# Performance work log

Measured on AMD Instinct MI355X. Metric: run time of the kernel, lower is better.

## Reference

```python
import jax, jax.numpy as jnp
import numpy as np

IN_FEATURES = 4096
OUT_FEATURES = 16384
BATCH, SEQ = 4, 2048


def setup_inputs() -> dict:
    key = jax.random.key(0)
    k_x, k_w, k_b = jax.random.split(key, 3)
    x = jax.random.normal(k_x, (BATCH, SEQ, IN_FEATURES), dtype=jnp.float32)
    # int8-valued quantized weight stored as int32 for portability (values in [-128, 127])
    weight_quantized = jax.random.randint(k_w, (OUT_FEATURES, IN_FEATURES), -128, 128, dtype=jnp.int32)
    weight_scale = jnp.float32(0.01)        # scalar scale (symmetric quant)
    weight_zero_point = jnp.float32(0.0)    # scalar zero point
    bias = jax.random.normal(k_b, (OUT_FEATURES,), dtype=jnp.float32)
    return {
        "x": x,
        "weight_quantized": weight_quantized,
        "weight_scale": weight_scale,
        "weight_zero_point": weight_zero_point,
        "bias": bias,
    }


def reference(x, weight_quantized, weight_scale, weight_zero_point, bias):
    # dequantize: (q - zero_point) * scale  -> fp32 weight [out, in]
    weight = (weight_quantized.astype(jnp.float32) - weight_zero_point) * weight_scale
    # F.linear: y = x @ W^T + b ; x: [b, s, in], W: [out, in] -> y: [b, s, out]
    return jnp.einsum("bsi,oi->bso", x, weight) + bias
```

## Files before the change

### kernel.cpp

```cpp
#include <hip/hip_runtime.h>
#include <hip/hip_bf16.h>
#include <cstdint>


#define M_DIM 8192
#define N_DIM 16384
#define K_DIM 4096
#define BK    128
#define NT    (K_DIM / BK)

using i32x4  = __attribute__((ext_vector_type(4))) int;
using i32x16 = __attribute__((ext_vector_type(16))) int;

__global__ __launch_bounds__(256) void quant_x_kernel(const float* __restrict__ x,
                                                      signed char* __restrict__ xq,
                                                      float* __restrict__ rs1,
                                                      float* __restrict__ rs2) {
    const int row = blockIdx.x;
    const float* xr = x + (size_t)row * K_DIM;
    const int tid = threadIdx.x;

    float4 v[4];
    float amax = 0.f;
    #pragma unroll
    for (int j = 0; j < 4; ++j) {
        v[j] = *(const float4*)(xr + j * 1024 + tid * 4);
        amax = fmaxf(amax, fmaxf(fmaxf(fabsf(v[j].x), fabsf(v[j].y)),
                                 fmaxf(fabsf(v[j].z), fabsf(v[j].w))));
    }
    #pragma unroll
    for (int off = 32; off > 0; off >>= 1)
        amax = fmaxf(amax, __shfl_xor(amax, off));
    __shared__ float smax[4];
    __shared__ int   ssum[4];
    const int wv = tid >> 6, ln = tid & 63;
    if (ln == 0) smax[wv] = amax;
    __syncthreads();
    amax = fmaxf(fmaxf(smax[0], smax[1]), fmaxf(smax[2], smax[3]));
    const float s   = amax * (1.0f / 127.0f);
    const float inv = amax > 0.f ? 127.0f / amax : 0.f;

    int sum = 0;
    #pragma unroll
    for (int j = 0; j < 4; ++j) {
        int q0 = (int)__builtin_rintf(v[j].x * inv);
        int q1 = (int)__builtin_rintf(v[j].y * inv);
        int q2 = (int)__builtin_rintf(v[j].z * inv);
        int q3 = (int)__builtin_rintf(v[j].w * inv);
        sum += q0 + q1 + q2 + q3;
        int packed = (q0 & 255) | ((q1 & 255) << 8) | ((q2 & 255) << 16) | ((q3 & 255) << 24);
        *(int*)(xq + (size_t)row * K_DIM + j * 1024 + tid * 4) = packed;
    }
    #pragma unroll
    for (int off = 32; off > 0; off >>= 1)
        sum += __shfl_xor(sum, off);
    if (ln == 0) ssum[wv] = sum;
    __syncthreads();
    if (tid == 0) {
        int t = ssum[0] + ssum[1] + ssum[2] + ssum[3];
        rs1[row] = s;
        rs2[row] = s * (float)t;
    }
}

__global__ void quant_w_kernel(const int* __restrict__ q, signed char* __restrict__ o,
                               long long n) {
    long long i = ((long long)blockIdx.x * blockDim.x + threadIdx.x) * 4;
    const long long stride = (long long)gridDim.x * blockDim.x * 4;
    for (; i < n; i += stride) {
        int4 v = *(const int4*)(q + i);
        int packed = (v.x & 255) | ((v.y & 255) << 8) | ((v.z & 255) << 16) | ((v.w & 255) << 24);
        *(int*)(o + i) = packed;
    }
}

#define SB() __builtin_amdgcn_sched_barrier(0)

__device__ __forceinline__ void barrier_() {
    SB();
    asm volatile("" ::: "memory");
    __builtin_amdgcn_s_barrier();
    asm volatile("" ::: "memory");
    SB();
}

__device__ __forceinline__ void stage_half8(const signed char* g0, unsigned char* l0) {
    __builtin_amdgcn_global_load_lds((const __attribute__((address_space(1))) void*)g0,
                                     (__attribute__((address_space(3))) void*)l0, 16, 0, 0);
    __builtin_amdgcn_global_load_lds(
        (const __attribute__((address_space(1))) void*)(g0 + (size_t)64 * K_DIM),
        (__attribute__((address_space(3))) void*)(l0 + 8192), 16, 0, 0);
}

__global__ __launch_bounds__(512, 2) void gemm_i8_kernel(const signed char* __restrict__ A,
                                                         const signed char* __restrict__ B,
                                                         const float* __restrict__ rs1,
                                                         const float* __restrict__ rs2,
                                                         const float* __restrict__ scale,
                                                         const float* __restrict__ zpp,
                                                         const float* __restrict__ bias,
                                                         float* __restrict__ C) {
    extern __shared__ unsigned char smem[];

    const int tid  = threadIdx.x;
    const int wave = tid >> 6;
    const int lane = tid & 63;
    const int fr = lane & 31, klo = lane >> 5;
    const int wr = wave >> 2, wc = wave & 3;

    const int nwg = (M_DIM / 256) * (N_DIM / 256);
    const int cpx = nwg >> 3;
    const int swz = (blockIdx.x & 7) * cpx + (blockIdx.x >> 3);
    const int ntn = N_DIM / 256;
    const int tileRow = (swz / ntn) * 256;
    const int tileCol = (swz % ntn) * 256;

    const size_t goff = (size_t)(tid >> 3) * K_DIM + (((tid & 7) ^ ((tid >> 3) & 7)) * 16);
    const signed char* Au  = A + (size_t)tileRow * K_DIM + goff;
    const signed char* Bu  = B + (size_t)tileCol * K_DIM + goff;
    const signed char* AuH = Au + (size_t)128 * K_DIM;
    const signed char* BuH = Bu + (size_t)128 * K_DIM;

    const int rA = wr * 128 + fr;
    const int rB = wc * 64 + fr;
    const int aoffB = rA * 128;
    const int boffB = 32768 + rB * 128;
    int cA[4], cB[4];
    #pragma unroll
    for (int ks = 0; ks < 4; ++ks) {
        cA[ks] = ((ks * 2 + klo) ^ (rA & 7)) * 16;
        cB[ks] = ((ks * 2 + klo) ^ (rB & 7)) * 16;
    }

    i32x16 acc[4][2] = {};
    i32x4 arA[2][4], arB[2][4], b0r[4], b1r[4];

    {
        unsigned char* w0 = smem + wave * 1024;
        unsigned char* w1 = smem + 65536 + wave * 1024;
        stage_half8(Au,  w0);
        stage_half8(AuH, w0 + 16384);
        stage_half8(Bu,  w0 + 32768);
        stage_half8(BuH, w0 + 49152);
        stage_half8(Bu + BK, w1 + 32768);
        stage_half8(Au + BK, w1);
    }
    SB();
    asm volatile("s_waitcnt vmcnt(4)" ::: "memory");
    barrier_();
    #pragma unroll
    for (int m = 0; m < 2; ++m)
        #pragma unroll
        for (int ks = 0; ks < 4; ++ks)
            arA[m][ks] = *(const i32x4*)(smem + aoffB + m * 4096 + cA[ks]);
    #pragma unroll
    for (int ks = 0; ks < 4; ++ks)
        b0r[ks] = *(const i32x4*)(smem + boffB + cB[ks]);
    SB();

    for (int t = 0; t < NT; ++t) {
        const unsigned char* sbr = smem + (t & 1) * 65536;
        const unsigned char* nxr = smem + ((t + 1) & 1) * 65536;
        unsigned char* sbw = smem + (t & 1) * 65536 + wave * 1024;
        unsigned char* nxw = smem + ((t + 1) & 1) * 65536 + wave * 1024;
        const int kn1 = (t + 1) * BK, kn2 = (t + 2) * BK;

        if (t + 1 < NT) stage_half8(AuH + kn1, nxw + 16384);
        #pragma unroll
        for (int ks = 0; ks < 4; ++ks)
            b1r[ks] = *(const i32x4*)(sbr + boffB + 4096 + cB[ks]);
        SB();
        asm volatile("s_waitcnt lgkmcnt(4)" ::: "memory");
        SB();
        __builtin_amdgcn_s_setprio(1);
        #pragma unroll
        for (int m = 0; m < 2; ++m)
            #pragma unroll
            for (int ks = 0; ks < 4; ++ks)
                acc[m][0] = __builtin_amdgcn_mfma_i32_32x32x32_i8(arA[m][ks], b0r[ks], acc[m][0], 0, 0, 0);
        __builtin_amdgcn_s_setprio(0);
        barrier_();

        if (t + 1 < NT) stage_half8(BuH + kn1, nxw + 49152);
        #pragma unroll
        for (int m = 0; m < 2; ++m)
            #pragma unroll
            for (int ks = 0; ks < 4; ++ks)
                arB[m][ks] = *(const i32x4*)(sbr + aoffB + (m + 2) * 4096 + cA[ks]);
        SB();
        asm volatile("s_waitcnt lgkmcnt(8)" ::: "memory");
        SB();
        __builtin_amdgcn_s_setprio(1);
        #pragma unroll
        for (int m = 0; m < 2; ++m)
            #pragma unroll
            for (int ks = 0; ks < 4; ++ks)
                acc[m][1] = __builtin_amdgcn_mfma_i32_32x32x32_i8(arA[m][ks], b1r[ks], acc[m][1], 0, 0, 0);
        __builtin_amdgcn_s_setprio(0);
        barrier_();

        if (t + 2 < NT) stage_half8(Bu + kn2, sbw + 32768);
        SB();
        asm volatile("s_waitcnt lgkmcnt(0)" ::: "memory");
        SB();
        __builtin_amdgcn_s_setprio(1);
        #pragma unroll
        for (int m = 0; m < 2; ++m)
            #pragma unroll
            for (int ks = 0; ks < 4; ++ks)
                acc[m + 2][1] = __builtin_amdgcn_mfma_i32_32x32x32_i8(arB[m][ks], b1r[ks], acc[m + 2][1], 0, 0, 0);
        __builtin_amdgcn_s_setprio(0);
        SB();
        if (t + 2 < NT) {
            asm volatile("s_waitcnt vmcnt(2)" ::: "memory");
        } else {
            asm volatile("s_waitcnt vmcnt(0)" ::: "memory");
        }
        barrier_();

        if (t + 1 < NT) {
            #pragma unroll
            for (int m = 0; m < 2; ++m)
                #pragma unroll
                for (int ks = 0; ks < 4; ++ks)
                    arA[m][ks] = *(const i32x4*)(nxr + aoffB + m * 4096 + cA[ks]);
        }
        if (t + 2 < NT) stage_half8(Au + kn2, sbw);
        SB();
        __builtin_amdgcn_s_setprio(1);
        #pragma unroll
        for (int m = 0; m < 2; ++m)
            #pragma unroll
            for (int ks = 0; ks < 4; ++ks)
                acc[m + 2][0] = __builtin_amdgcn_mfma_i32_32x32x32_i8(arB[m][ks], b0r[ks], acc[m + 2][0], 0, 0, 0);
        __builtin_amdgcn_s_setprio(0);
        if (t + 1 < NT) {
            #pragma unroll
            for (int ks = 0; ks < 4; ++ks)
                b0r[ks] = *(const i32x4*)(nxr + boffB + cB[ks]);
        }
        SB();
        barrier_();
    }

    const float sw  = scale[0];
    const float zpv = zpp[0];
    const float bv0 = bias[tileCol + wc * 64 + fr];
    const float bv1 = bias[tileCol + wc * 64 + 32 + fr];
    #pragma unroll
    for (int m = 0; m < 4; ++m) {
        #pragma unroll
        for (int r = 0; r < 16; ++r) {
            const int grow = tileRow + wr * 128 + m * 32 + (r & 3) + 8 * (r >> 2) + 4 * klo;
            const float f1 = rs1[grow] * sw;
            const float f2 = zpv * rs2[grow] * sw;
            const int gc0 = tileCol + wc * 64 + fr;
            C[(size_t)grow * N_DIM + gc0]      = f1 * (float)acc[m][0][r] - f2 + bv0;
            C[(size_t)grow * N_DIM + gc0 + 32] = f1 * (float)acc[m][1][r] - f2 + bv1;
        }
    }
}

__global__ void gemm_naive(const float* __restrict__ x, const int* __restrict__ wq,
                           const float* __restrict__ sp, const float* __restrict__ zp,
                           const float* __restrict__ bias, float* __restrict__ out) {
    __shared__ float sX[32][33];
    __shared__ float sW[32][33];
    const float s = sp[0], z = zp[0];
    const int tx = threadIdx.x & 15, ty = threadIdx.x >> 4;
    const int row0 = blockIdx.y * 32, col0 = blockIdx.x * 32;
    float acc[2][2] = {};
    for (int k0 = 0; k0 < K_DIM; k0 += 32) {
        for (int i = threadIdx.x; i < 32 * 32; i += 256) {
            int r = i >> 5, c = i & 31;
            sX[r][c] = x[(size_t)(row0 + r) * K_DIM + k0 + c];
            sW[r][c] = ((float)wq[(size_t)(col0 + r) * K_DIM + k0 + c] - z) * s;
        }
        __syncthreads();
        #pragma unroll
        for (int k = 0; k < 32; ++k) {
            float xa0 = sX[ty * 2][k], xa1 = sX[ty * 2 + 1][k];
            float wb0 = sW[tx * 2][k], wb1 = sW[tx * 2 + 1][k];
            acc[0][0] += xa0 * wb0; acc[0][1] += xa0 * wb1;
            acc[1][0] += xa1 * wb0; acc[1][1] += xa1 * wb1;
        }
        __syncthreads();
    }
    #pragma unroll
    for (int i = 0; i < 2; ++i)
        #pragma unroll
        for (int j = 0; j < 2; ++j)
            out[(size_t)(row0 + ty * 2 + i) * N_DIM + (col0 + tx * 2 + j)] =
                acc[i][j] + bias[col0 + tx * 2 + j];
}

extern "C" void kernel_launch(void* const* d_in, const int* in_sizes, int n_in,
                              void* d_out, int out_size, void* d_ws, size_t ws_size,
                              hipStream_t stream) {
    const float* x     = (const float*)d_in[0];
    const int*   wq    = (const int*)d_in[1];
    const float* scale = (const float*)d_in[2];
    const float* zp    = (const float*)d_in[3];
    const float* bias  = (const float*)d_in[4];
    float* out = (float*)d_out;

    const size_t offXq = 0;
    const size_t offWq = (size_t)M_DIM * K_DIM;
    const size_t offR1 = offWq + (size_t)N_DIM * K_DIM;
    const size_t offR2 = offR1 + (size_t)M_DIM * sizeof(float);
    const size_t need  = offR2 + (size_t)M_DIM * sizeof(float);

    if (ws_size >= need) {
        signed char* xq  = (signed char*)d_ws + offXq;
        signed char* wq8 = (signed char*)d_ws + offWq;
        float* rs1 = (float*)((char*)d_ws + offR1);
        float* rs2 = (float*)((char*)d_ws + offR2);
        quant_x_kernel<<<M_DIM, 256, 0, stream>>>(x, xq, rs1, rs2);
        quant_w_kernel<<<4096, 256, 0, stream>>>(wq, wq8, (long long)N_DIM * K_DIM);
        (void)hipFuncSetAttribute((const void*)gemm_i8_kernel,
                                  hipFuncAttributeMaxDynamicSharedMemorySize, 131072);
        gemm_i8_kernel<<<(M_DIM / 256) * (N_DIM / 256), 512, 131072, stream>>>(
            xq, wq8, rs1, rs2, scale, zp, bias, out);
    } else {
        dim3 grid(N_DIM / 32, M_DIM / 32);
        gemm_naive<<<grid, 256, 0, stream>>>(x, wq, scale, zp, bias, out);
    }
}
```

Measured before the change: 684.9 us.

## Use 4-wave workgroups with 128x128 per-wave tiles in int8 GEMM

Halves the workgroup from 512 to 256 threads, so each wave computes a 128x128 output subtile (4x4 MFMA accumulators) instead of 128x64. Each LDS fragment load now feeds more MFMAs, raising register-level reuse and cutting LDS read traffic per FLOP, and each thread issues four async global-to-LDS loads per stage. The tile-to-block swizzle is also changed to walk rows first within each column group. The cost is doubled accumulator registers, which limits occupancy to one workgroup per CU and leaves fewer waves to hide latency.

Measured after the change: 767.4 us. 12.0% more time.

```diff
diff --git a/kernel.cpp b/kernel.cpp
--- a/kernel.cpp
+++ b/kernel.cpp
@@ -84,15 +84,15 @@
     SB();
 }
 
-__device__ __forceinline__ void stage_half8(const signed char* g0, unsigned char* l0) {
-    __builtin_amdgcn_global_load_lds((const __attribute__((address_space(1))) void*)g0,
-                                     (__attribute__((address_space(3))) void*)l0, 16, 0, 0);
-    __builtin_amdgcn_global_load_lds(
-        (const __attribute__((address_space(1))) void*)(g0 + (size_t)64 * K_DIM),
-        (__attribute__((address_space(3))) void*)(l0 + 8192), 16, 0, 0);
-}
-
-__global__ __launch_bounds__(512, 2) void gemm_i8_kernel(const signed char* __restrict__ A,
+__device__ __forceinline__ void stage_half4(const signed char* g0, unsigned char* l0) {
+    #pragma unroll
+    for (int j = 0; j < 4; ++j)
+        __builtin_amdgcn_global_load_lds(
+            (const __attribute__((address_space(1))) void*)(g0 + (size_t)(j * 32) * K_DIM),
+            (__attribute__((address_space(3))) void*)(l0 + j * 4096), 16, 0, 0);
+}
+
+__global__ __launch_bounds__(256, 1) void gemm_i8_kernel(const signed char* __restrict__ A,
                                                          const signed char* __restrict__ B,
                                                          const float* __restrict__ rs1,
                                                          const float* __restrict__ rs2,
@@ -106,14 +106,11 @@
     const int wave = tid >> 6;
     const int lane = tid & 63;
     const int fr = lane & 31, klo = lane >> 5;
-    const int wr = wave >> 2, wc = wave & 3;
-
-    const int nwg = (M_DIM / 256) * (N_DIM / 256);
-    const int cpx = nwg >> 3;
-    const int swz = (blockIdx.x & 7) * cpx + (blockIdx.x >> 3);
-    const int ntn = N_DIM / 256;
-    const int tileRow = (swz / ntn) * 256;
-    const int tileCol = (swz % ntn) * 256;
+    const int wr = wave >> 1, wc = wave & 1;
+
+    const int swz = (blockIdx.x & 7) * 256 + (blockIdx.x >> 3);
+    const int tileRow = (swz & 31) * 256;
+    const int tileCol = (swz >> 5) * 256;
 
     const size_t goff = (size_t)(tid >> 3) * K_DIM + (((tid & 7) ^ ((tid >> 3) & 7)) * 16);
     const signed char* Au  = A + (size_t)tileRow * K_DIM + goff;
@@ -121,41 +118,39 @@
     const signed char* AuH = Au + (size_t)128 * K_DIM;
     const signed char* BuH = Bu + (size_t)128 * K_DIM;
 
-    const int rA = wr * 128 + fr;
-    const int rB = wc * 64 + fr;
-    const int aoffB = rA * 128;
-    const int boffB = 32768 + rB * 128;
-    int cA[4], cB[4];
-    #pragma unroll
-    for (int ks = 0; ks < 4; ++ks) {
-        cA[ks] = ((ks * 2 + klo) ^ (rA & 7)) * 16;
-        cB[ks] = ((ks * 2 + klo) ^ (rB & 7)) * 16;
-    }
-
-    i32x16 acc[4][2] = {};
-    i32x4 arA[2][4], arB[2][4], b0r[4], b1r[4];
+    const int aoffB = wr * 16384 + fr * 128;
+    const int boffB = 32768 + wc * 16384 + fr * 128;
+    int c[4];
+    #pragma unroll
+    for (int ks = 0; ks < 4; ++ks)
+        c[ks] = ((ks * 2 + klo) ^ (fr & 7)) * 16;
+
+    i32x16 acc[4][4] = {};
+    i32x4 arA[2][4], arB[2][4], b0r[2][4], b1r[2][4];
 
     {
         unsigned char* w0 = smem + wave * 1024;
         unsigned char* w1 = smem + 65536 + wave * 1024;
-        stage_half8(Au,  w0);
-        stage_half8(AuH, w0 + 16384);
-        stage_half8(Bu,  w0 + 32768);
-        stage_half8(BuH, w0 + 49152);
-        stage_half8(Bu + BK, w1 + 32768);
-        stage_half8(Au + BK, w1);
+        stage_half4(Au,  w0);
+        stage_half4(AuH, w0 + 16384);
+        stage_half4(Bu,  w0 + 32768);
+        stage_half4(BuH, w0 + 49152);
+        stage_half4(Bu + BK, w1 + 32768);
+        stage_half4(Au + BK, w1);
     }
     SB();
-    asm volatile("s_waitcnt vmcnt(4)" ::: "memory");
+    asm volatile("s_waitcnt vmcnt(8)" ::: "memory");
     barrier_();
     #pragma unroll
     for (int m = 0; m < 2; ++m)
         #pragma unroll
         for (int ks = 0; ks < 4; ++ks)
-            arA[m][ks] = *(const i32x4*)(smem + aoffB + m * 4096 + cA[ks]);
-    #pragma unroll
-    for (int ks = 0; ks < 4; ++ks)
-        b0r[ks] = *(const i32x4*)(smem + boffB + cB[ks]);
+            arA[m][ks] = *(const i32x4*)(smem + aoffB + m * 4096 + c[ks]);
+    #pragma unroll
+    for (int n = 0; n < 2; ++n)
+        #pragma unroll
+        for (int ks = 0; ks < 4; ++ks)
+            b0r[n][ks] = *(const i32x4*)(smem + boffB + n * 4096 + c[ks]);
     SB();
 
     for (int t = 0; t < NT; ++t) {
@@ -165,55 +160,63 @@
         unsigned char* nxw = smem + ((t + 1) & 1) * 65536 + wave * 1024;
         const int kn1 = (t + 1) * BK, kn2 = (t + 2) * BK;
 
-        if (t + 1 < NT) stage_half8(AuH + kn1, nxw + 16384);
-        #pragma unroll
-        for (int ks = 0; ks < 4; ++ks)
-            b1r[ks] = *(const i32x4*)(sbr + boffB + 4096 + cB[ks]);
-        SB();
-        asm volatile("s_waitcnt lgkmcnt(4)" ::: "memory");
+        if (t + 1 < NT) stage_half4(AuH + kn1, nxw + 16384);
+        #pragma unroll
+        for (int n = 0; n < 2; ++n)
+            #pragma unroll
+            for (int ks = 0; ks < 4; ++ks)
+                b1r[n][ks] = *(const i32x4*)(sbr + boffB + (n + 2) * 4096 + c[ks]);
+        SB();
+        asm volatile("s_waitcnt lgkmcnt(8)" ::: "memory");
         SB();
         __builtin_amdgcn_s_setprio(1);
         #pragma unroll
-        for (int m = 0; m < 2; ++m)
-            #pragma unroll
-            for (int ks = 0; ks < 4; ++ks)
-                acc[m][0] = __builtin_amdgcn_mfma_i32_32x32x32_i8(arA[m][ks], b0r[ks], acc[m][0], 0, 0, 0);
+        for (int ks = 0; ks < 4; ++ks)
+            #pragma unroll
+            for (int m = 0; m < 2; ++m)
+                #pragma unroll
+                for (int n = 0; n < 2; ++n)
+                    acc[m][n] = __builtin_amdgcn_mfma_i32_32x32x32_i8(arA[m][ks], b0r[n][ks], acc[m][n], 0, 0, 0);
         __builtin_amdgcn_s_setprio(0);
         barrier_();
 
-        if (t + 1 < NT) stage_half8(BuH + kn1, nxw + 49152);
+        if (t + 1 < NT) stage_half4(BuH + kn1, nxw + 49152);
         #pragma unroll
         for (int m = 0; m < 2; ++m)
             #pragma unroll
             for (int ks = 0; ks < 4; ++ks)
-                arB[m][ks] = *(const i32x4*)(sbr + aoffB + (m + 2) * 4096 + cA[ks]);
+                arB[m][ks] = *(const i32x4*)(sbr + aoffB + (m + 2) * 4096 + c[ks]);
         SB();
         asm volatile("s_waitcnt lgkmcnt(8)" ::: "memory");
         SB();
         __builtin_amdgcn_s_setprio(1);
         #pragma unroll
-        for (int m = 0; m < 2; ++m)
-            #pragma unroll
-            for (int ks = 0; ks < 4; ++ks)
-                acc[m][1] = __builtin_amdgcn_mfma_i32_32x32x32_i8(arA[m][ks], b1r[ks], acc[m][1], 0, 0, 0);
+        for (int ks = 0; ks < 4; ++ks)
+            #pragma unroll
+            for (int m = 0; m < 2; ++m)
+                #pragma unroll
+                for (int n = 0; n < 2; ++n)
+                    acc[m][n + 2] = __builtin_amdgcn_mfma_i32_32x32x32_i8(arA[m][ks], b1r[n][ks], acc[m][n + 2], 0, 0, 0);
         __builtin_amdgcn_s_setprio(0);
         barrier_();
 
-        if (t + 2 < NT) stage_half8(Bu + kn2, sbw + 32768);
+        if (t + 2 < NT) stage_half4(Bu + kn2, sbw + 32768);
         SB();
         asm volatile("s_waitcnt lgkmcnt(0)" ::: "memory");
         SB();
         __builtin_amdgcn_s_setprio(1);
         #pragma unroll
-        for (int m = 0; m < 2; ++m)
-            #pragma unroll
-            for (int ks = 0; ks < 4; ++ks)
-                acc[m + 2][1] = __builtin_amdgcn_mfma_i32_32x32x32_i8(arB[m][ks], b1r[ks], acc[m + 2][1], 0, 0, 0);
+        for (int ks = 0; ks < 4; ++ks)
+            #pragma unroll
+            for (int m = 0; m < 2; ++m)
+                #pragma unroll
+                for (int n = 0; n < 2; ++n)
+                    acc[m + 2][n + 2] = __builtin_amdgcn_mfma_i32_32x32x32_i8(arB[m][ks], b1r[n][ks], acc[m + 2][n + 2], 0, 0, 0);
         __builtin_amdgcn_s_setprio(0);
         SB();
         if (t + 2 < NT) {
-            asm volatile("s_waitcnt vmcnt(2)" ::: "memory");
-        } else {
+            asm volatile("s_waitcnt vmcnt(4)" ::: "memory");
+        } else if (t + 1 < NT) {
             asm volatile("s_waitcnt vmcnt(0)" ::: "memory");
         }
         barrier_();
@@ -223,21 +226,25 @@
             for (int m = 0; m < 2; ++m)
                 #pragma unroll
                 for (int ks = 0; ks < 4; ++ks)
-                    arA[m][ks] = *(const i32x4*)(nxr + aoffB + m * 4096 + cA[ks]);
-        }
-        if (t + 2 < NT) stage_half8(Au + kn2, sbw);
+                    arA[m][ks] = *(const i32x4*)(nxr + aoffB + m * 4096 + c[ks]);
+        }
+        if (t + 2 < NT) stage_half4(Au + kn2, sbw);
         SB();
         __builtin_amdgcn_s_setprio(1);
         #pragma unroll
-        for (int m = 0; m < 2; ++m)
-            #pragma unroll
-            for (int ks = 0; ks < 4; ++ks)
-                acc[m + 2][0] = __builtin_amdgcn_mfma_i32_32x32x32_i8(arB[m][ks], b0r[ks], acc[m + 2][0], 0, 0, 0);
+        for (int ks = 0; ks < 4; ++ks)
+            #pragma unroll
+            for (int m = 0; m < 2; ++m)
+                #pragma unroll
+                for (int n = 0; n < 2; ++n)
+                    acc[m + 2][n] = __builtin_amdgcn_mfma_i32_32x32x32_i8(arB[m][ks], b0r[n][ks], acc[m + 2][n], 0, 0, 0);
         __builtin_amdgcn_s_setprio(0);
         if (t + 1 < NT) {
             #pragma unroll
-            for (int ks = 0; ks < 4; ++ks)
-                b0r[ks] = *(const i32x4*)(nxr + boffB + cB[ks]);
+            for (int n = 0; n < 2; ++n)
+                #pragma unroll
+                for (int ks = 0; ks < 4; ++ks)
+                    b0r[n][ks] = *(const i32x4*)(nxr + boffB + n * 4096 + c[ks]);
         }
         SB();
         barrier_();
@@ -245,8 +252,10 @@
 
     const float sw  = scale[0];
     const float zpv = zpp[0];
-    const float bv0 = bias[tileCol + wc * 64 + fr];
-    const float bv1 = bias[tileCol + wc * 64 + 32 + fr];
+    float bv[4];
+    #pragma unroll
+    for (int n = 0; n < 4; ++n)
+        bv[n] = bias[tileCol + wc * 128 + n * 32 + fr];
     #pragma unroll
     for (int m = 0; m < 4; ++m) {
         #pragma unroll
@@ -254,9 +263,10 @@
             const int grow = tileRow + wr * 128 + m * 32 + (r & 3) + 8 * (r >> 2) + 4 * klo;
             const float f1 = rs1[grow] * sw;
             const float f2 = zpv * rs2[grow] * sw;
-            const int gc0 = tileCol + wc * 64 + fr;
-            C[(size_t)grow * N_DIM + gc0]      = f1 * (float)acc[m][0][r] - f2 + bv0;
-            C[(size_t)grow * N_DIM + gc0 + 32] = f1 * (float)acc[m][1][r] - f2 + bv1;
+            float* Crow = C + (size_t)grow * N_DIM + tileCol + wc * 128 + fr;
+            #pragma unroll
+            for (int n = 0; n < 4; ++n)
+                Crow[n * 32] = f1 * (float)acc[m][n][r] - f2 + bv[n];
         }
     }
 }
@@ -272,9 +282,9 @@
     float acc[2][2] = {};
     for (int k0 = 0; k0 < K_DIM; k0 += 32) {
         for (int i = threadIdx.x; i < 32 * 32; i += 256) {
-            int r = i >> 5, c = i & 31;
-            sX[r][c] = x[(size_t)(row0 + r) * K_DIM + k0 + c];
-            sW[r][c] = ((float)wq[(size_t)(col0 + r) * K_DIM + k0 + c] - z) * s;
+            int r = i >> 5, cc2 = i & 31;
+            sX[r][cc2] = x[(size_t)(row0 + r) * K_DIM + k0 + cc2];
+            sW[r][cc2] = ((float)wq[(size_t)(col0 + r) * K_DIM + k0 + cc2] - z) * s;
         }
         __syncthreads();
         #pragma unroll
@@ -319,7 +329,7 @@
         quant_w_kernel<<<4096, 256, 0, stream>>>(wq, wq8, (long long)N_DIM * K_DIM);
         (void)hipFuncSetAttribute((const void*)gemm_i8_kernel,
                                   hipFuncAttributeMaxDynamicSharedMemorySize, 131072);
-        gemm_i8_kernel<<<(M_DIM / 256) * (N_DIM / 256), 512, 131072, stream>>>(
+        gemm_i8_kernel<<<(M_DIM / 256) * (N_DIM / 256), 256, 131072, stream>>>(
             xq, wq8, rs1, rs2, scale, zp, bias, out);
     } else {
         dim3 grid(N_DIM / 32, M_DIM / 32);
```
